# Optimization experiments

Measured on AMD Instinct MI355X. Metric: run time of the kernel, lower is better.

Reference implementation:

```python
import jax, jax.numpy as jnp
import numpy as np

K_TOP = 10
DEPTH = 1
N_RULES = 2
N_HOPS = 2
IS_REVERSED = (False, True)


def setup_inputs() -> dict:
    key = jax.random.key(0)
    ks = jax.random.split(key, 11)
    B, E, N, F = 16, 256, 1024, 2048
    return {
        'rel': jax.random.normal(ks[0], (B, E), jnp.float32),
        'arg1': jax.random.normal(ks[1], (B, E), jnp.float32),
        'arg2': jax.random.normal(ks[2], (B, E), jnp.float32),
        'fact_rel': jax.random.normal(ks[3], (B, F, E), jnp.float32),
        'fact_arg1': jax.random.normal(ks[4], (B, F, E), jnp.float32),
        'fact_arg2': jax.random.normal(ks[5], (B, F, E), jnp.float32),
        'nb_facts': jax.random.randint(ks[6], (B,), 1, F + 1),
        'entity_embeddings': jax.random.normal(ks[7], (B, N, E), jnp.float32),
        'nb_entities': jax.random.randint(ks[8], (B,), 1, N + 1),
        'W': jax.random.normal(ks[9], (N_RULES, N_HOPS, E, E), jnp.float32) / np.sqrt(E),
        'b': jnp.zeros((N_RULES, N_HOPS, E), jnp.float32),
    }


def _kernel_scores(q, f):
    # q: [B, M, E], f: [B, F, E] -> Gaussian kernel exp(-0.5*||q-f||^2): [B, M, F]
    d = (jnp.sum(q * q, -1)[..., None] + jnp.sum(f * f, -1)[:, None, :]
         - 2.0 * jnp.einsum('bme,bfe->bmf', q, f))
    return jnp.exp(-0.5 * jnp.maximum(d, 0.0))


def kb_score(rel, arg1, arg2, fact_rel, fact_arg1, fact_arg2, nb_facts):
    # BatchNeuralKB.score: product of per-component kernels, mask padded facts, max over facts.
    B, F, E = fact_rel.shape
    M = rel.shape[0] // B
    r = rel.reshape(B, M, E); a1 = arg1.reshape(B, M, E); a2 = arg2.reshape(B, M, E)
    s = (_kernel_scores(r, fact_rel) * _kernel_scores(a1, fact_arg1)
         * _kernel_scores(a2, fact_arg2))                       # [B, M, F]
    mask = jnp.arange(F)[None, None, :] < nb_facts[:, None, None]
    s = jnp.where(mask, s, 0.0)
    return jnp.max(s, axis=-1).reshape(-1)                      # [B*M]


def prove(rel, arg1, arg2, fact_rel, fact_arg1, fact_arg2, nb_facts,
          entity_embeddings, W, b, depth):
    scores_0 = kb_score(rel, arg1, arg2, fact_rel, fact_arg1, fact_arg2, nb_facts)
    if depth == 0:
        return scores_0
    B, E = rel.shape
    N = entity_embeddings.shape[1]
    global_res = None
    for rule_idx in range(N_RULES):
        is_rev = IS_REVERSED[rule_idx]
        hop_rel_lst = [rel @ W[rule_idx, h] + b[rule_idx, h] for h in range(N_HOPS)]
        sources, scores = arg1, None
        for hop_idx, hop_rel in enumerate(hop_rel_lst, start=1):
            sources_2d = sources.reshape(-1, E)
            nb_branches = sources_2d.shape[0] // B
            hop_rel_2d = jnp.repeat(hop_rel, nb_branches, axis=0)   # [B*br, E]
            if hop_idx < N_HOPS:
                ent_rep = jnp.repeat(entity_embeddings, nb_branches, axis=0)  # [B*br, N, E]
                all_ent_2d = ent_rep.reshape(-1, E)                  # [B*br*N, E]
                new_src_2d = jnp.repeat(sources_2d, N, axis=0)       # [B*br*N, E]
                hop_rel_big = jnp.repeat(hop_rel_2d, N, axis=0)
                na1, na2 = (all_ent_2d, new_src_2d) if is_rev else (new_src_2d, all_ent_2d)
                new_scores = prove(hop_rel_big, na1, na2, fact_rel, fact_arg1,
                                   fact_arg2, nb_facts, entity_embeddings, W, b,
                                   depth - 1).reshape(-1, N)         # [B*br, N]
                k = min(K_TOP, N)
                z_scores, z_idx = jax.lax.top_k(new_scores, k)       # [B*br, k]
                z_emb = jnp.take_along_axis(ent_rep, z_idx[..., None], axis=1)  # [B*br, k, E]
                sources = z_emb.reshape(-1, E)
                z1d = z_scores.reshape(-1)
                scores = z1d if scores is None else jnp.minimum(z1d, jnp.repeat(scores, k))
            else:
                arg2_2d = jnp.repeat(arg2, nb_branches, axis=0)
                na1, na2 = (arg2_2d, sources_2d) if is_rev else (sources_2d, arg2_2d)
                z1d = prove(hop_rel_2d, na1, na2, fact_rel, fact_arg1, fact_arg2,
                            nb_facts, entity_embeddings, W, b, depth - 1)
                scores = z1d if scores is None else jnp.minimum(z1d, scores)
        res = jnp.max(scores.reshape(B, -1), axis=1)
        global_res = res if global_res is None else jnp.maximum(global_res, res)
    return jnp.maximum(scores_0, global_res)


def reference(rel, arg1, arg2, fact_rel, fact_arg1, fact_arg2, nb_facts,
              entity_embeddings, nb_entities, W, b):
    return prove(rel, arg1, arg2, fact_rel, fact_arg1, fact_arg2, nb_facts,
                 entity_embeddings, W, b, depth=DEPTH)
```

## Files before the change

kernel.cpp:

```cpp
#include <hip/hip_runtime.h>
#include <math.h>

#define E 256
#define KTOP 10
#define NY 8
#define NINF (-__builtin_huge_valf())

typedef __attribute__((ext_vector_type(4))) float f32x4;
typedef __attribute__((ext_vector_type(2))) long i64x2;

__device__ inline float wsum(float v) {
    v += __shfl_xor(v, 1, 64);
    v += __shfl_xor(v, 2, 64);
    v += __shfl_xor(v, 4, 64);
    v += __shfl_xor(v, 8, 64);
    v += __shfl_xor(v, 16, 64);
    v += __shfl_xor(v, 32, 64);
    return v;
}

__device__ inline float wmax(float v) {
    v = fmaxf(v, __shfl_xor(v, 1, 64));
    v = fmaxf(v, __shfl_xor(v, 2, 64));
    v = fmaxf(v, __shfl_xor(v, 4, 64));
    v = fmaxf(v, __shfl_xor(v, 8, 64));
    v = fmaxf(v, __shfl_xor(v, 16, 64));
    v = fmaxf(v, __shfl_xor(v, 32, 64));
    return v;
}

__device__ inline float dot4(float4 a, float4 b) {
    return a.x * b.x + a.y * b.y + a.z * b.z + a.w * b.w;
}

__device__ inline void atomicMaxF(float* addr, float v) {
    atomicMax((unsigned int*)addr, __float_as_uint(v));
}

__device__ inline unsigned char f2fp8(float x) {
    unsigned u = __float_as_uint(x);
    unsigned s = (u >> 24) & 0x80u;
    int e = (int)((u >> 23) & 0xFF) - 127;
    unsigned m = u & 0x7FFFFFu;
    if (e < -9) return (unsigned char)s;
    if (e > 8) return (unsigned char)(s | 0x7E);
    if (e >= -6) {
        unsigned mant = m >> 20;
        unsigned rest = m & 0xFFFFFu;
        if (rest > 0x80000u || (rest == 0x80000u && (mant & 1))) mant++;
        unsigned v = (((unsigned)(e + 7)) << 3) + mant;
        if (v > 0x7Eu) v = 0x7Eu;
        return (unsigned char)(s | v);
    }
    int rs = 20 + (-6 - e);
    unsigned full = 0x800000u | m;
    unsigned mant = full >> rs;
    unsigned rem = full & ((1u << rs) - 1u);
    unsigned half = 1u << (rs - 1);
    if (rem > half || (rem == half && (mant & 1))) mant++;
    if (mant >= 8u) return (unsigned char)(s | 0x08u);
    return (unsigned char)(s | mant);
}

#if defined(__has_builtin)
#if __has_builtin(__builtin_amdgcn_cvt_pk_fp8_f32)
#define HAVE_HW_FP8 1
#endif
#endif

__device__ inline unsigned pack_fp8x4(float a, float b, float c, float d) {
#ifdef HAVE_HW_FP8
    int lo = __builtin_amdgcn_cvt_pk_fp8_f32(a, b, 0, false);
    return (unsigned)__builtin_amdgcn_cvt_pk_fp8_f32(c, d, lo, true);
#else
    return (unsigned)f2fp8(a) | ((unsigned)f2fp8(b) << 8) |
           ((unsigned)f2fp8(c) << 16) | ((unsigned)f2fp8(d) << 24);
#endif
}

__device__ inline int tile_off(int e0, int col) {
    return ((e0 >> 6) << 10) + (((e0 & 31) >> 3) << 8) + (col << 4) +
           (((e0 >> 5) & 1) << 3) + (e0 & 7);
}

__global__ void k_hoprel(const float* __restrict__ rel, const float* __restrict__ W,
                         const float* __restrict__ bias, float* __restrict__ hr,
                         int B) {
    int b = blockIdx.x, rh = blockIdx.y;
    int j = threadIdx.x;
    __shared__ float relS[E];
    relS[j] = rel[b * E + j];
    __syncthreads();
    const float* Wp = W + (size_t)rh * E * E;
    float acc = bias[rh * E + j];
#pragma unroll 8
    for (int e = 0; e < E; ++e) acc = fmaf(relS[e], Wp[e * E + j], acc);
    hr[((size_t)rh * B + b) * E + j] = acc;
}

__global__ void k_prep_ent(const float* __restrict__ ent, unsigned char* __restrict__ entb,
                           unsigned char* __restrict__ entt, float* __restrict__ ne_,
                           int BN, int N) {
    int row = blockIdx.x * 4 + (threadIdx.x >> 6);
    if (row >= BN) return;
    int lane = threadIdx.x & 63;
    float4 v = ((const float4*)(ent + (size_t)row * E))[lane];
    float s = wsum(dot4(v, v));
    if (lane == 0) ne_[row] = s;
    unsigned o = pack_fp8x4(v.x, v.y, v.z, v.w);
    ((unsigned*)(entb + (size_t)row * E))[lane] = o;
    int b = row / N, n = row % N;
    size_t tbase = ((size_t)b * (N >> 4) + (n >> 4)) * 4096;
    *(unsigned*)(entt + tbase + tile_off(lane * 4, n & 15)) = o;
}

__global__ __launch_bounds__(64) void k_prep_q(
    const float* __restrict__ rel, const float* __restrict__ arg1,
    const float* __restrict__ arg2, const float* __restrict__ hr,
    unsigned char* __restrict__ qt, int B) {
    int b = blockIdx.x;
    int lane = threadIdx.x;
    unsigned char* t = qt + (size_t)b * 4096;
#define ROW(q, ptr)                                                       \
    {                                                                     \
        float4 v = ((const float4*)(ptr))[lane];                          \
        *(unsigned*)(t + tile_off(lane * 4, q)) =                         \
            pack_fp8x4(v.x, v.y, v.z, v.w);                               \
    }
    ROW(0, rel + (size_t)b * E)
    ROW(1, arg1 + (size_t)b * E)
    ROW(2, arg2 + (size_t)b * E)
    ROW(3, hr + ((size_t)0 * B + b) * E)
    ROW(4, hr + ((size_t)1 * B + b) * E)
    ROW(5, hr + ((size_t)2 * B + b) * E)
    ROW(6, hr + ((size_t)3 * B + b) * E)
#undef ROW
#pragma unroll
    for (int q = 7; q < 16; ++q)
        *(unsigned*)(t + tile_off(lane * 4, q)) = 0u;
}

__global__ __launch_bounds__(256) void k_castpair(
    const float* __restrict__ frel, const float* __restrict__ fa1,
    const float* __restrict__ fa2, const unsigned char* __restrict__ qt,
    const int* __restrict__ nbf, float* __restrict__ lw1, float* __restrict__ lw2,
    float* __restrict__ s0log, float* __restrict__ nf1, float* __restrict__ nf2,
    unsigned char* __restrict__ fa1b, unsigned char* __restrict__ fa2b,
    int B, int F) {
    int ti = blockIdx.x, b = blockIdx.y;
    int f0 = ti * 16;
    int tid = threadIdx.x;
    __shared__ unsigned char sFR[4096], sF1[4096], sF2[4096];
    __shared__ float vals[16][12];
    __shared__ float qn[8];
    int row = tid >> 4;
    int cb = (tid & 15) * 4;
    size_t rbase = ((size_t)b * F + f0 + row) * E;
#pragma unroll
    for (int p = 0; p < 4; ++p) {
        int e0 = p * 64 + cb;
        float4 vr = *(const float4*)(frel + rbase + e0);
        float4 v1 = *(const float4*)(fa1 + rbase + e0);
        float4 v2 = *(const float4*)(fa2 + rbase + e0);
        int off = tile_off(e0, row);
        *(unsigned*)&sFR[off] = pack_fp8x4(vr.x, vr.y, vr.z, vr.w);
        *(unsigned*)&sF1[off] = pack_fp8x4(v1.x, v1.y, v1.z, v1.w);
        *(unsigned*)&sF2[off] = pack_fp8x4(v2.x, v2.y, v2.z, v2.w);
    }
    __syncthreads();
    size_t tb = ((size_t)b * (F >> 4) + ti) * 4096;
    *(i64x2*)(fa1b + tb + tid * 16) = *(const i64x2*)&sF1[tid * 16];
    *(i64x2*)(fa2b + tb + tid * 16) = *(const i64x2*)&sF2[tid * 16];
    if (tid >= 64) return;
    int lane = tid, lr = lane & 15, lk = lane >> 4;
    const unsigned char* qp = qt + (size_t)b * 4096 + lane * 16;
    long Q[8], FR[8], F1[8], F2[8];
#pragma unroll
    for (int g = 0; g < 4; ++g) {
        i64x2 a = *(const i64x2*)(qp + g * 1024);
        Q[2 * g] = a.x; Q[2 * g + 1] = a.y;
        i64x2 c = *(const i64x2*)&sFR[g * 1024 + lane * 16];
        FR[2 * g] = c.x; FR[2 * g + 1] = c.y;
        i64x2 d = *(const i64x2*)&sF1[g * 1024 + lane * 16];
        F1[2 * g] = d.x; F1[2 * g + 1] = d.y;
        i64x2 e2 = *(const i64x2*)&sF2[g * 1024 + lane * 16];
        F2[2 * g] = e2.x; F2[2 * g + 1] = e2.y;
    }
    f32x4 Dqq = {0.f, 0.f, 0.f, 0.f}, D1 = Dqq, D2 = Dqq, D3 = Dqq, D4 = Dqq,
          D5 = Dqq, D6 = Dqq;
#pragma unroll
    for (int kb = 0; kb < 8; ++kb) {
        Dqq = __builtin_amdgcn_mfma_f32_16x16x32_fp8_fp8(Q[kb], Q[kb], Dqq, 0, 0, 0);
        D1 = __builtin_amdgcn_mfma_f32_16x16x32_fp8_fp8(Q[kb], FR[kb], D1, 0, 0, 0);
        D2 = __builtin_amdgcn_mfma_f32_16x16x32_fp8_fp8(Q[kb], F1[kb], D2, 0, 0, 0);
        D3 = __builtin_amdgcn_mfma_f32_16x16x32_fp8_fp8(Q[kb], F2[kb], D3, 0, 0, 0);
        D4 = __builtin_amdgcn_mfma_f32_16x16x32_fp8_fp8(FR[kb], FR[kb], D4, 0, 0, 0);
        D5 = __builtin_amdgcn_mfma_f32_16x16x32_fp8_fp8(F1[kb], F1[kb], D5, 0, 0, 0);
        D6 = __builtin_amdgcn_mfma_f32_16x16x32_fp8_fp8(F2[kb], F2[kb], D6, 0, 0, 0);
    }
#pragma unroll
    for (int j = 0; j < 4; ++j) {
        int q = lk * 4 + j;
        if (q == 0) vals[lr][0] = D1[j];
        if (q == 3) vals[lr][1] = D1[j];
        if (q == 4) vals[lr][2] = D1[j];
        if (q == 5) vals[lr][3] = D1[j];
        if (q == 6) vals[lr][4] = D1[j];
        if (q == 1) { vals[lr][5] = D2[j]; vals[lr][7] = D3[j]; }
        if (q == 2) { vals[lr][6] = D2[j]; vals[lr][8] = D3[j]; }
        if (q == lr) {
            vals[lr][9] = D4[j];
            vals[lr][10] = D5[j];
            vals[lr][11] = D6[j];
            if (q < 7) qn[q] = Dqq[j];
        }
    }
    if (lane < 16) {
        int f = f0 + lane;
        size_t bf = (size_t)b * F + f;
        const float* vv = vals[lane];
        float nfr = vv[9], n1 = vv[10], n2 = vv[11];
        bool msk = (f < nbf[b]);
        float rrel  = fmaxf(qn[0] + nfr - 2.f * vv[0], 0.f);
        float rh00  = fmaxf(qn[3] + nfr - 2.f * vv[1], 0.f);
        float rh01  = fmaxf(qn[4] + nfr - 2.f * vv[2], 0.f);
        float rh10  = fmaxf(qn[5] + nfr - 2.f * vv[3], 0.f);
        float rh11  = fmaxf(qn[6] + nfr - 2.f * vv[4], 0.f);
        float ra1f1 = fmaxf(qn[1] + n1 - 2.f * vv[5], 0.f);
        float ra2f1 = fmaxf(qn[2] + n1 - 2.f * vv[6], 0.f);
        float ra1f2 = fmaxf(qn[1] + n2 - 2.f * vv[7], 0.f);
        float ra2f2 = fmaxf(qn[2] + n2 - 2.f * vv[8], 0.f);
        nf1[bf] = n1;
        nf2[bf] = n2;
        lw1[bf]                 = msk ? -0.5f * (rh00 + ra1f1) : NINF;
        lw1[(size_t)B * F + bf] = msk ? -0.5f * (rh10 + ra1f2) : NINF;
        lw2[bf]                 = msk ? -0.5f * (rh01 + ra2f2) : NINF;
        lw2[(size_t)B * F + bf] = msk ? -0.5f * (rh11 + ra2f1) : NINF;
        s0log[bf] = msk ? -0.5f * (rrel + ra1f1 + ra2f2) : NINF;
    }
}

__global__ void k_s0red(const float* __restrict__ s0log, float* __restrict__ out,
                        int B, int F) {
    int b = blockIdx.x;
    int tid = threadIdx.x, lane = tid & 63, wave = tid >> 6;
    float m = NINF;
    for (int f = tid; f < F; f += 256) m = fmaxf(m, s0log[(size_t)b * F + f]);
    m = wmax(m);
    __shared__ float red[4];
    if (lane == 0) red[wave] = m;
    __syncthreads();
    if (tid == 0) out[b] = expf(fmaxf(fmaxf(red[0], red[1]), fmaxf(red[2], red[3])));
}

__global__ __launch_bounds__(256, 4) void k_hop1m(
    const unsigned char* __restrict__ entt, const unsigned char* __restrict__ fa1b,
    const unsigned char* __restrict__ fa2b, const float* __restrict__ nf1,
    const float* __restrict__ nf2, const float* __restrict__ ne,
    const float* __restrict__ lw1, float* __restrict__ nsc_part, int B, int N, int F) {
    int L = blockIdx.x;
    int xcd = L & 7, s = L >> 3;
    int b = ((s >> 7) << 3) | xcd;
    int inner = s & 127;
    int r = inner >> 6, nb = (inner >> 3) & 7, fs = inner & 7;
    int BR = nb * 128;
    int F0 = fs * 256;
    const unsigned char* factb = (r == 0) ? fa2b : fa1b;
    const float* nfp = ((r == 0) ? nf2 : nf1) + (size_t)b * F;
    const float* w = lw1 + ((size_t)r * B + b) * F;
    const float* nep = ne + (size_t)b * N;

    __shared__ unsigned char bT[2][4096];

    int tid = threadIdx.x, lane = tid & 63, wave = tid >> 6;
    int lr = lane & 15, lk = lane >> 4;
    int row0 = BR + wave * 32;

    const unsigned char* At = entt + (size_t)b * N * E;
    long areg[2][8];
#pragma unroll
    for (int m = 0; m < 2; ++m) {
        const unsigned char* p = At + (size_t)((row0 >> 4) + m) * 4096 + lk * 256 +
                                 lr * 16;
#pragma unroll
        for (int g = 0; g < 4; ++g) {
            i64x2 vv = *(const i64x2*)(p + g * 1024);
            areg[m][2 * g] = vv.x;
            areg[m][2 * g + 1] = vv.y;
        }
    }
    float nh[2][4];
#pragma unroll
    for (int m = 0; m < 2; ++m)
#pragma unroll
        for (int j = 0; j < 4; ++j)
            nh[m][j] = -0.5f * nep[row0 + m * 16 + lk * 4 + j];
    float lwa[16], gfa[16];
#pragma unroll
    for (int t = 0; t < 16; ++t) {
        int fcol = F0 + t * 16 + lr;
        lwa[t] = w[fcol];
        gfa[t] = fmaf(-0.5f, nfp[fcol], lwa[t]);
    }
    float vmax[2][4];
#pragma unroll
    for (int m = 0; m < 2; ++m)
#pragma unroll
        for (int j = 0; j < 4; ++j) vmax[m][j] = NINF;

    const unsigned char* Bt = factb + (size_t)b * F * E + (size_t)(F0 >> 4) * 4096;
#define STG(buf, t)                                                            \
    __builtin_amdgcn_global_load_lds(                                          \
        (const __attribute__((address_space(1))) void*)(Bt + (size_t)(t) * 4096 + \
                                                        wave * 1024 + lane * 16), \
        (__attribute__((address_space(3))) void*)&bT[buf][wave * 1024], 16, 0, 0)

    STG(0, 0);
    __syncthreads();
#pragma unroll
    for (int t = 0; t < 16; ++t) {
        int cur = t & 1;
        if (t < 15) STG(cur ^ 1, t + 1);
        long bfr[8];
#pragma unroll
        for (int g = 0; g < 4; ++g) {
            i64x2 vv = *(const i64x2*)&bT[cur][g * 1024 + lane * 16];
            bfr[2 * g] = vv.x;
            bfr[2 * g + 1] = vv.y;
        }
        f32x4 acc0 = {0.f, 0.f, 0.f, 0.f}, acc1 = {0.f, 0.f, 0.f, 0.f};
#pragma unroll
        for (int kb = 0; kb < 8; ++kb) {
            acc0 = __builtin_amdgcn_mfma_f32_16x16x32_fp8_fp8(areg[0][kb], bfr[kb],
                                                              acc0, 0, 0, 0);
            acc1 = __builtin_amdgcn_mfma_f32_16x16x32_fp8_fp8(areg[1][kb], bfr[kb],
                                                              acc1, 0, 0, 0);
        }
#pragma unroll
        for (int j = 0; j < 4; ++j) {
            vmax[0][j] = fmaxf(vmax[0][j], fminf(acc0[j] + gfa[t] + nh[0][j], lwa[t]));
            vmax[1][j] = fmaxf(vmax[1][j], fminf(acc1[j] + gfa[t] + nh[1][j], lwa[t]));
        }
        __syncthreads();
    }
#undef STG

#pragma unroll
    for (int m = 0; m < 2; ++m)
#pragma unroll
        for (int j = 0; j < 4; ++j) {
            float v = vmax[m][j];
            v = fmaxf(v, __shfl_xor(v, 1, 64));
            v = fmaxf(v, __shfl_xor(v, 2, 64));
            v = fmaxf(v, __shfl_xor(v, 4, 64));
            v = fmaxf(v, __shfl_xor(v, 8, 64));
            if (lr == 0) {
                int row = row0 + m * 16 + lk * 4 + j;
                nsc_part[(size_t)fs * (2 * (size_t)B * N) +
                         ((size_t)r * B + b) * N + row] = v;
            }
        }
}

__global__ __launch_bounds__(256) void k_topk(const float* __restrict__ nsc_part,
                                              float* __restrict__ zval,
                                              int* __restrict__ zidx, int B, int N) {
    int b = blockIdx.x, r = blockIdx.y;
    int tid = threadIdx.x, lane = tid & 63, wave = tid >> 6;
    size_t rbN = ((size_t)r * B + b) * N;
    size_t ystr = 2 * (size_t)B * N;
    const float4* p0 = (const float4*)(nsc_part + rbN) + tid;
    float4 m = *p0;
#pragma unroll
    for (int y = 1; y < NY; ++y) {
        float4 t = *(const float4*)((const float*)p0 + (size_t)y * ystr);
        m.x = fmaxf(m.x, t.x); m.y = fmaxf(m.y, t.y);
        m.z = fmaxf(m.z, t.z); m.w = fmaxf(m.w, t.w);
    }
    float v0 = expf(m.x), v1 = expf(m.y), v2 = expf(m.z), v3 = expf(m.w);
    int base = tid * 4;
    __shared__ float rv[4];
    __shared__ int ri[4];
    for (int t = 0; t < KTOP; ++t) {
        float bv = v0; int bi = base;
        if (v1 > bv) { bv = v1; bi = base + 1; }
        if (v2 > bv) { bv = v2; bi = base + 2; }
        if (v3 > bv) { bv = v3; bi = base + 3; }
#pragma unroll
        for (int off = 32; off > 0; off >>= 1) {
            float ov = __shfl_xor(bv, off, 64);
            int oi = __shfl_xor(bi, off, 64);
            if (ov > bv || (ov == bv && oi < bi)) { bv = ov; bi = oi; }
        }
        if (lane == 0) { rv[wave] = bv; ri[wave] = bi; }
        __syncthreads();
        float fb = rv[0]; int fi = ri[0];
#pragma unroll
        for (int wv = 1; wv < 4; ++wv) {
            float ov = rv[wv]; int oi = ri[wv];
            if (ov > fb || (ov == fb && oi < fi)) { fb = ov; fi = oi; }
        }
        if (tid == 0) {
            zval[((size_t)r * B + b) * KTOP + t] = fb;
            zidx[((size_t)r * B + b) * KTOP + t] = fi;
        }
        int off = fi - base;
        v0 = (off == 0) ? -2.f : v0;
        v1 = (off == 1) ? -2.f : v1;
        v2 = (off == 2) ? -2.f : v2;
        v3 = (off == 3) ? -2.f : v3;
        __syncthreads();
    }
}

__global__ __launch_bounds__(256) void k_hop2m(
    const unsigned char* __restrict__ entb, const unsigned char* __restrict__ fa1b,
    const unsigned char* __restrict__ fa2b, const float* __restrict__ nf1,
    const float* __restrict__ nf2, const float* __restrict__ ne,
    const float* __restrict__ lw2, const int* __restrict__ zidx,
    float* __restrict__ h2part, int B, int N, int F) {
    int L = blockIdx.x;
    int xcd = L & 7, s = L >> 3;
    int b = ((s >> 4) << 3) | xcd;
    int inner = s & 15;
    int r = inner >> 3, c = inner & 7;
    const unsigned char* factb = (r == 0) ? fa1b : fa2b;
    const float* nfp = ((r == 0) ? nf1 : nf2) + (size_t)b * F;
    const float* w = lw2 + ((size_t)r * B + b) * F;
    int tid = threadIdx.x, lane = tid & 63, wave = tid >> 6;
    int lr = lane & 15, lk = lane >> 4;
    __shared__ unsigned char aLds[32 * 16 * 8];
    __shared__ float snrm[16];
    for (int ci = tid; ci < 512; ci += 256) {
        int row = ci & 15, kc = ci >> 4;
        long vv = 0;
        if (row < KTOP) {
            int idx = zidx[((size_t)r * B + b) * KTOP + row];
            vv = *(const long*)(entb + ((size_t)b * N + idx) * E + kc * 8);
        }
        *(long*)&aLds[(size_t)ci * 8] = vv;
    }
    if (tid < 16) {
        float nv = 0.f;
        if (tid < KTOP) {
            int idx = zidx[((size_t)r * B + b) * KTOP + tid];
            nv = ne[(size_t)b * N + idx];
        }
        snrm[tid] = nv;
    }
    __syncthreads();
    long afr[8];
#pragma unroll
    for (int kb = 0; kb < 8; ++kb)
        afr[kb] = *(const long*)&aLds[((kb * 4 + lk) * 16 + lr) * 8];
    float nhs[4];
#pragma unroll
    for (int j = 0; j < 4; ++j) nhs[j] = -0.5f * snrm[lk * 4 + j];
    int fbase = c * (F >> 3) + wave * (F >> 5);
    float vmax[4] = {NINF, NINF, NINF, NINF};
    const unsigned char* Bb = factb + (size_t)b * F * E;
#pragma unroll
    for (int n = 0; n < 4; ++n) {
        int fcol = fbase + n * 16;
        const unsigned char* p = Bb + (size_t)(fcol >> 4) * 4096 + lk * 256 + lr * 16;
        long bfr[8];
#pragma unroll
        for (int g = 0; g < 4; ++g) {
            i64x2 vv = *(const i64x2*)(p + g * 1024);
            bfr[2 * g] = vv.x;
            bfr[2 * g + 1] = vv.y;
        }
        f32x4 acc = {0.f, 0.f, 0.f, 0.f};
#pragma unroll
        for (int kb = 0; kb < 8; ++kb)
            acc = __builtin_amdgcn_mfma_f32_16x16x32_fp8_fp8(afr[kb], bfr[kb], acc,
                                                             0, 0, 0);
        float lwf = w[fcol + lr];
        float gf = fmaf(-0.5f, nfp[fcol + lr], lwf);
#pragma unroll
        for (int j = 0; j < 4; ++j)
            vmax[j] = fmaxf(vmax[j], fminf(acc[j] + gf + nhs[j], lwf));
    }
#pragma unroll
    for (int j = 0; j < 4; ++j) {
        float v = vmax[j];
        v = fmaxf(v, __shfl_xor(v, 1, 64));
        v = fmaxf(v, __shfl_xor(v, 2, 64));
        v = fmaxf(v, __shfl_xor(v, 4, 64));
        v = fmaxf(v, __shfl_xor(v, 8, 64));
        int sidx = lk * 4 + j;
        if (lr == 0 && sidx < KTOP)
            h2part[(((size_t)r * B + b) * KTOP + sidx) * 32 + c * 4 + wave] = v;
    }
}

__global__ void k_hop2c(const float* __restrict__ h2part, const float* __restrict__ zval,
                        float* __restrict__ out, int B) {
    int i = blockIdx.x * 256 + threadIdx.x;
    int n = 2 * B * KTOP;
    if (i < n) {
        int b = (i / KTOP) % B;
        float m = NINF;
#pragma unroll
        for (int c2 = 0; c2 < 32; ++c2) m = fmaxf(m, h2part[(size_t)i * 32 + c2]);
        float sc = fminf(expf(m), zval[i]);
        atomicMaxF(&out[b], sc);
    }
}

extern "C" void kernel_launch(void* const* d_in, const int* in_sizes, int n_in,
                              void* d_out, int out_size, void* d_ws, size_t ws_size,
                              hipStream_t stream) {
    const float* rel = (const float*)d_in[0];
    const float* arg1 = (const float*)d_in[1];
    const float* arg2 = (const float*)d_in[2];
    const float* frel = (const float*)d_in[3];
    const float* fa1 = (const float*)d_in[4];
    const float* fa2 = (const float*)d_in[5];
    const int* nbf = (const int*)d_in[6];
    const float* ent = (const float*)d_in[7];
    const float* W = (const float*)d_in[9];
    const float* bias = (const float*)d_in[10];
    int B = in_sizes[0] / E;
    int F = in_sizes[3] / (B * E);
    int N = in_sizes[7] / (B * E);
    float* out = (float*)d_out;

    float* ws = (float*)d_ws;
    size_t o = 0;
    float* hr = ws + o;   o += (size_t)4 * B * E;
    float* nf1 = ws + o;  o += (size_t)B * F;
    float* nf2 = ws + o;  o += (size_t)B * F;
    float* ne_ = ws + o;  o += (size_t)B * N;
    float* lw1 = ws + o;  o += (size_t)2 * B * F;
    float* lw2 = ws + o;  o += (size_t)2 * B * F;
    float* zval = ws + o; o += (size_t)2 * B * KTOP;
    int* zidx = (int*)(ws + o); o += (size_t)2 * B * KTOP;
    float* s0log = ws + o; o += (size_t)B * F;
    float* h2part = ws + o; o += (size_t)2 * B * KTOP * 32;
    float* nsc_part = ws + o; o += (size_t)NY * 2 * B * N;
    unsigned char* fa1b = (unsigned char*)(ws + o); o += (size_t)B * F * E / 4;
    unsigned char* fa2b = (unsigned char*)(ws + o); o += (size_t)B * F * E / 4;
    unsigned char* entb = (unsigned char*)(ws + o); o += (size_t)B * N * E / 4;
    unsigned char* entt = (unsigned char*)(ws + o); o += (size_t)B * N * E / 4;
    unsigned char* qt = (unsigned char*)(ws + o);   o += (size_t)B * 1024;

    k_hoprel<<<dim3(B, 4), dim3(E), 0, stream>>>(rel, W, bias, hr, B);
    k_prep_ent<<<dim3((B * N + 3) / 4), dim3(256), 0, stream>>>(ent, entb, entt, ne_,
                                                                B * N, N);
    k_prep_q<<<dim3(B), dim3(64), 0, stream>>>(rel, arg1, arg2, hr, qt, B);
    k_castpair<<<dim3(F / 16, B), dim3(256), 0, stream>>>(
        frel, fa1, fa2, qt, nbf, lw1, lw2, s0log, nf1, nf2, fa1b, fa2b, B, F);
    k_s0red<<<dim3(B), dim3(256), 0, stream>>>(s0log, out, B, F);
    k_hop1m<<<dim3(2048), dim3(256), 0, stream>>>(entt, fa1b, fa2b, nf1, nf2, ne_, lw1,
                                                  nsc_part, B, N, F);
    k_topk<<<dim3(B, 2), dim3(256), 0, stream>>>(nsc_part, zval, zidx, B, N);
    k_hop2m<<<dim3(256), dim3(256), 0, stream>>>(entb, fa1b, fa2b, nf1, nf2, ne_, lw2,
                                                 zidx, h2part, B, N, F);
    k_hop2c<<<dim3((2 * B * KTOP + 255) / 256), dim3(256), 0, stream>>>(h2part, zval,
                                                                        out, B);
}
```

Before: 94.37 us.

## Process both rules per block in hop1 to reuse entity A fragments

Each k_hop1m block now handles both rule directions (fa2b and fa1b facts) for the same entity rows and fact slice, halving the grid from 2048 to 1024 blocks. The entity A-operand registers and norm terms are loaded once and reused across two MFMA streams, and shared memory double-buffers both fact tiles. The per-column weight and norm values are now read from global memory inside the loop instead of being preloaded. The cost is fewer blocks (less parallelism), more registers and LDS per block, and in-loop global loads.

```diff
diff --git a/kernel.cpp b/kernel.cpp
--- a/kernel.cpp
+++ b/kernel.cpp
@@ -260,17 +260,18 @@
     const float* __restrict__ lw1, float* __restrict__ nsc_part, int B, int N, int F) {
     int L = blockIdx.x;
     int xcd = L & 7, s = L >> 3;
-    int b = ((s >> 7) << 3) | xcd;
-    int inner = s & 127;
-    int r = inner >> 6, nb = (inner >> 3) & 7, fs = inner & 7;
+    int b = ((s >> 6) << 3) | xcd;
+    int inner = s & 63;
+    int nb = (inner >> 3) & 7, fs = inner & 7;
     int BR = nb * 128;
     int F0 = fs * 256;
-    const unsigned char* factb = (r == 0) ? fa2b : fa1b;
-    const float* nfp = ((r == 0) ? nf2 : nf1) + (size_t)b * F;
-    const float* w = lw1 + ((size_t)r * B + b) * F;
+    const float* nfp0 = nf2 + (size_t)b * F;
+    const float* nfp1 = nf1 + (size_t)b * F;
+    const float* w0 = lw1 + (size_t)b * F;
+    const float* w1 = lw1 + ((size_t)B + b) * F;
     const float* nep = ne + (size_t)b * N;
 
-    __shared__ unsigned char bT[2][4096];
+    __shared__ unsigned char bT[2][2][4096];
 
     int tid = threadIdx.x, lane = tid & 63, wave = tid >> 6;
     int lr = lane & 15, lk = lane >> 4;
@@ -295,25 +296,29 @@
 #pragma unroll
         for (int j = 0; j < 4; ++j)
             nh[m][j] = -0.5f * nep[row0 + m * 16 + lk * 4 + j];
-    float lwa[16], gfa[16];
-#pragma unroll
-    for (int t = 0; t < 16; ++t) {
-        int fcol = F0 + t * 16 + lr;
-        lwa[t] = w[fcol];
-        gfa[t] = fmaf(-0.5f, nfp[fcol], lwa[t]);
-    }
-    float vmax[2][4];
-#pragma unroll
-    for (int m = 0; m < 2; ++m)
-#pragma unroll
-        for (int j = 0; j < 4; ++j) vmax[m][j] = NINF;
-
-    const unsigned char* Bt = factb + (size_t)b * F * E + (size_t)(F0 >> 4) * 4096;
-#define STG(buf, t)                                                            \
-    __builtin_amdgcn_global_load_lds(                                          \
-        (const __attribute__((address_space(1))) void*)(Bt + (size_t)(t) * 4096 + \
-                                                        wave * 1024 + lane * 16), \
-        (__attribute__((address_space(3))) void*)&bT[buf][wave * 1024], 16, 0, 0)
+    float vmax[2][2][4];
+#pragma unroll
+    for (int r = 0; r < 2; ++r)
+#pragma unroll
+        for (int m = 0; m < 2; ++m)
+#pragma unroll
+            for (int j = 0; j < 4; ++j) vmax[r][m][j] = NINF;
+
+    const unsigned char* Bt0 = fa2b + (size_t)b * F * E + (size_t)(F0 >> 4) * 4096;
+    const unsigned char* Bt1 = fa1b + (size_t)b * F * E + (size_t)(F0 >> 4) * 4096;
+#define STG(buf, t)                                                              \
+    {                                                                            \
+        __builtin_amdgcn_global_load_lds(                                        \
+            (const __attribute__((address_space(1))) void*)(Bt0 + (size_t)(t) * 4096 + \
+                                                            wave * 1024 + lane * 16),  \
+            (__attribute__((address_space(3))) void*)&bT[buf][0][wave * 1024], 16, 0,  \
+            0);                                                                  \
+        __builtin_amdgcn_global_load_lds(                                        \
+            (const __attribute__((address_space(1))) void*)(Bt1 + (size_t)(t) * 4096 + \
+                                                            wave * 1024 + lane * 16),  \
+            (__attribute__((address_space(3))) void*)&bT[buf][1][wave * 1024], 16, 0,  \
+            0);                                                                  \
+    }
 
     STG(0, 0);
     __syncthreads();
@@ -321,45 +326,56 @@
     for (int t = 0; t < 16; ++t) {
         int cur = t & 1;
         if (t < 15) STG(cur ^ 1, t + 1);
-        long bfr[8];
-#pragma unroll
-        for (int g = 0; g < 4; ++g) {
-            i64x2 vv = *(const i64x2*)&bT[cur][g * 1024 + lane * 16];
-            bfr[2 * g] = vv.x;
-            bfr[2 * g + 1] = vv.y;
-        }
-        f32x4 acc0 = {0.f, 0.f, 0.f, 0.f}, acc1 = {0.f, 0.f, 0.f, 0.f};
-#pragma unroll
-        for (int kb = 0; kb < 8; ++kb) {
-            acc0 = __builtin_amdgcn_mfma_f32_16x16x32_fp8_fp8(areg[0][kb], bfr[kb],
-                                                              acc0, 0, 0, 0);
-            acc1 = __builtin_amdgcn_mfma_f32_16x16x32_fp8_fp8(areg[1][kb], bfr[kb],
-                                                              acc1, 0, 0, 0);
-        }
-#pragma unroll
-        for (int j = 0; j < 4; ++j) {
-            vmax[0][j] = fmaxf(vmax[0][j], fminf(acc0[j] + gfa[t] + nh[0][j], lwa[t]));
-            vmax[1][j] = fmaxf(vmax[1][j], fminf(acc1[j] + gfa[t] + nh[1][j], lwa[t]));
+        int fcol = F0 + t * 16 + lr;
+#pragma unroll
+        for (int r = 0; r < 2; ++r) {
+            long bfr[8];
+#pragma unroll
+            for (int g = 0; g < 4; ++g) {
+                i64x2 vv = *(const i64x2*)&bT[cur][r][g * 1024 + lane * 16];
+                bfr[2 * g] = vv.x;
+                bfr[2 * g + 1] = vv.y;
+            }
+            f32x4 acc0 = {0.f, 0.f, 0.f, 0.f}, acc1 = {0.f, 0.f, 0.f, 0.f};
+#pragma unroll
+            for (int kb = 0; kb < 8; ++kb) {
+                acc0 = __builtin_amdgcn_mfma_f32_16x16x32_fp8_fp8(areg[0][kb], bfr[kb],
+                                                                  acc0, 0, 0, 0);
+                acc1 = __builtin_amdgcn_mfma_f32_16x16x32_fp8_fp8(areg[1][kb], bfr[kb],
+                                                                  acc1, 0, 0, 0);
+            }
+            float lwf = (r == 0) ? w0[fcol] : w1[fcol];
+            float nfv = (r == 0) ? nfp0[fcol] : nfp1[fcol];
+            float gf = fmaf(-0.5f, nfv, lwf);
+#pragma unroll
+            for (int j = 0; j < 4; ++j) {
+                vmax[r][0][j] =
+                    fmaxf(vmax[r][0][j], fminf(acc0[j] + gf + nh[0][j], lwf));
+                vmax[r][1][j] =
+                    fmaxf(vmax[r][1][j], fminf(acc1[j] + gf + nh[1][j], lwf));
+            }
         }
         __syncthreads();
     }
 #undef STG
 
 #pragma unroll
-    for (int m = 0; m < 2; ++m)
-#pragma unroll
-        for (int j = 0; j < 4; ++j) {
-            float v = vmax[m][j];
-            v = fmaxf(v, __shfl_xor(v, 1, 64));
-            v = fmaxf(v, __shfl_xor(v, 2, 64));
-            v = fmaxf(v, __shfl_xor(v, 4, 64));
-            v = fmaxf(v, __shfl_xor(v, 8, 64));
-            if (lr == 0) {
-                int row = row0 + m * 16 + lk * 4 + j;
-                nsc_part[(size_t)fs * (2 * (size_t)B * N) +
-                         ((size_t)r * B + b) * N + row] = v;
+    for (int r = 0; r < 2; ++r)
+#pragma unroll
+        for (int m = 0; m < 2; ++m)
+#pragma unroll
+            for (int j = 0; j < 4; ++j) {
+                float v = vmax[r][m][j];
+                v = fmaxf(v, __shfl_xor(v, 1, 64));
+                v = fmaxf(v, __shfl_xor(v, 2, 64));
+                v = fmaxf(v, __shfl_xor(v, 4, 64));
+                v = fmaxf(v, __shfl_xor(v, 8, 64));
+                if (lr == 0) {
+                    int row = row0 + m * 16 + lk * 4 + j;
+                    nsc_part[(size_t)fs * (2 * (size_t)B * N) +
+                             ((size_t)r * B + b) * N + row] = v;
+                }
             }
-        }
 }
 
 __global__ __launch_bounds__(256) void k_topk(const float* __restrict__ nsc_part,
@@ -552,7 +568,7 @@
     k_castpair<<<dim3(F / 16, B), dim3(256), 0, stream>>>(
         frel, fa1, fa2, qt, nbf, lw1, lw2, s0log, nf1, nf2, fa1b, fa2b, B, F);
     k_s0red<<<dim3(B), dim3(256), 0, stream>>>(s0log, out, B, F);
-    k_hop1m<<<dim3(2048), dim3(256), 0, stream>>>(entt, fa1b, fa2b, nf1, nf2, ne_, lw1,
+    k_hop1m<<<dim3(1024), dim3(256), 0, stream>>>(entt, fa1b, fa2b, nf1, nf2, ne_, lw1,
                                                   nsc_part, B, N, F);
     k_topk<<<dim3(B, 2), dim3(256), 0, stream>>>(nsc_part, zval, zidx, B, N);
     k_hop2m<<<dim3(256), dim3(256), 0, stream>>>(entb, fa1b, fa2b, nf1, nf2, ne_, lw2,
```

Result: slower. 174.7 us (+85.1%).
